# Kernel optimization log

Measured on AMD Instinct MI355X. Metric: run time of the kernel, lower is better.

Reference implementation:

```python
import jax, jax.numpy as jnp
import numpy as np

NUM_USERS = 1_000_000
NUM_AGES = 8
NUM_ATTR = 40
FACE_K = 64
VISUAL_DIM = 2048
HIDDEN = 512
BATCH = 16384
VOCAB = NUM_USERS + 24 + 2 + NUM_AGES + NUM_ATTR  # fm_linear input width


def setup_inputs() -> dict:
    key = jax.random.key(0)
    ks = jax.random.split(key, 24)
    s = 0.02
    inp = {
        "user_id": jax.random.randint(ks[0], (BATCH,), 0, NUM_USERS),
        "hour": jax.random.randint(ks[1], (BATCH,), 0, 24),
        "visual": jax.random.normal(ks[2], (BATCH, VISUAL_DIM), jnp.float32),
        "scale": jax.random.uniform(ks[3], (BATCH, 1), jnp.float32),
        "gender": jax.random.randint(ks[4], (BATCH,), 0, 2),
        "age": jax.random.randint(ks[5], (BATCH,), 0, NUM_AGES),
        "attribute": jax.random.randint(ks[6], (BATCH,), 0, NUM_ATTR),
        # embedding tables
        "user_emb": jax.random.normal(ks[7], (NUM_USERS, FACE_K), jnp.float32) * s,
        "hour_emb": jax.random.normal(ks[8], (24, FACE_K), jnp.float32) * s,
        "gender_emb": jax.random.normal(ks[9], (2, FACE_K), jnp.float32) * s,
        "age_emb": jax.random.normal(ks[10], (NUM_AGES, FACE_K), jnp.float32) * s,
        "attr_emb": jax.random.normal(ks[11], (NUM_ATTR, FACE_K), jnp.float32) * s,
        # visual linear
        "visu_w": jax.random.normal(ks[12], (FACE_K, VISUAL_DIM), jnp.float32) * s,
        "visu_b": jnp.zeros((FACE_K,), jnp.float32),
        # fm linear over concatenated one-hots (width VOCAB, out 2)
        "fm_w": jax.random.normal(ks[13], (2, VOCAB), jnp.float32) * s,
        "fm_b": jnp.zeros((2,), jnp.float32),
        # dnn
        "w1": jax.random.normal(ks[14], (HIDDEN, 6 * FACE_K), jnp.float32) * s,
        "b1": jnp.zeros((HIDDEN,), jnp.float32),
        "w2": jax.random.normal(ks[15], (HIDDEN, HIDDEN), jnp.float32) * s,
        "b2": jnp.zeros((HIDDEN,), jnp.float32),
        "w3": jax.random.normal(ks[16], (2, HIDDEN), jnp.float32) * s,
        "b3": jnp.zeros((2,), jnp.float32),
    }
    return inp


def reference(user_id, hour, visual, scale, gender, age, attribute,
              user_emb, hour_emb, gender_emb, age_emb, attr_emb,
              visu_w, visu_b, fm_w, fm_b, w1, b1, w2, b2, w3, b3):
    B = user_id.shape[0]
    # fm linear: one_hot @ W^T == gather-sum of W columns at the hot indices
    cols = jnp.stack([
        user_id,
        NUM_USERS + hour,
        NUM_USERS + 24 + gender,
        NUM_USERS + 24 + 2 + age,
        NUM_USERS + 24 + 2 + NUM_AGES + attribute,
    ], axis=1)  # [B, 5]
    linear_part = fm_w[:, cols].sum(axis=2).T + fm_b  # [B, 2]

    # embeddings
    user = user_emb[user_id]            # [B, K]
    hr = hour_emb[hour]                 # [B, K]
    face = jnp.stack([gender_emb[gender], attr_emb[attribute], age_emb[age]], axis=1)  # [B,3,K]
    face = scale[:, None, :] * jnp.tanh(face)  # scale [B,1] -> [B,1,1]
    embeddings = jnp.concatenate([user[:, None, :], hr[:, None, :], face], axis=1)  # [B,5,K]

    # FM second order
    so = jnp.square(embeddings.sum(axis=1)) - jnp.square(embeddings).sum(axis=1)  # [B,K]
    second_order = 0.5 * so.sum(axis=1)  # [B]
    fm = linear_part + second_order[:, None]  # [B,2]

    # DNN
    vis = visual @ visu_w.T + visu_b  # [B,K]
    x = jnp.concatenate([embeddings.reshape(B, 5 * FACE_K), vis], axis=1)  # [B,6K]
    x = jax.nn.relu(x @ w1.T + b1)
    x = jax.nn.relu(x @ w2.T + b2)
    x = x @ w3.T + b3
    return jax.nn.softmax(fm + x, axis=1)
```

## Files before the change

### kernel.cpp

```cpp
#include <hip/hip_runtime.h>
#include <hip/hip_bf16.h>
#include <stdint.h>

#define BATCH 16384
#define FACE_K 64
#define VISUAL_DIM 2048
#define HIDDEN 512
#define NUM_USERS 1000000
#define NUM_AGES 8
#define NUM_ATTR 40
#define VOCAB (NUM_USERS + 24 + 2 + NUM_AGES + NUM_ATTR)
#define XDIM 384

typedef __bf16 bf16x8 __attribute__((ext_vector_type(8)));
typedef float f32x4 __attribute__((ext_vector_type(4)));

__device__ __forceinline__ uint16_t f2bf(float f) {
    union { float f; uint32_t u; } v; v.f = f;
    uint32_t r = v.u + 0x7fffu + ((v.u >> 16) & 1u);
    return (uint16_t)(r >> 16);
}
__device__ __forceinline__ float bf2f(uint16_t h) {
    union { uint32_t u; float f; } v; v.u = ((uint32_t)h) << 16;
    return v.f;
}

__global__ void cvt_all(const float* __restrict__ visu_w, const float* __restrict__ w1,
                        const float* __restrict__ w2, uint16_t* __restrict__ vwb,
                        uint16_t* __restrict__ w1b, uint16_t* __restrict__ w2b) {
    int i = blockIdx.x * blockDim.x + threadIdx.x;
    const float4* src;
    ushort4* dst;
    if (i < 32768)       { src = (const float4*)visu_w + i;        dst = (ushort4*)vwb + i; }
    else if (i < 81920)  { src = (const float4*)w1 + (i - 32768);  dst = (ushort4*)w1b + (i - 32768); }
    else                 { src = (const float4*)w2 + (i - 81920);  dst = (ushort4*)w2b + (i - 81920); }
    float4 v = *src;
    ushort4 o;
    o.x = f2bf(v.x); o.y = f2bf(v.y); o.z = f2bf(v.z); o.w = f2bf(v.w);
    *dst = o;
}

#define VIS_BLOCKS 1024
__global__ __launch_bounds__(256) void front_kernel(
        const float* __restrict__ visual, const uint16_t* __restrict__ Wb,
        const float* __restrict__ bias,
        const int* __restrict__ uid, const int* __restrict__ hour,
        const float* __restrict__ scale, const int* __restrict__ gender,
        const int* __restrict__ age, const int* __restrict__ attr,
        const float* __restrict__ user_emb, const float* __restrict__ hour_emb,
        const float* __restrict__ gender_emb, const float* __restrict__ age_emb,
        const float* __restrict__ attr_emb,
        const float* __restrict__ fm_w, const float* __restrict__ fm_b,
        uint16_t* __restrict__ x, float* __restrict__ fm) {
    __shared__ float red[3 * 64 * 17];
    int t = threadIdx.x;
    int wv = t >> 6, lane = t & 63;

    if (blockIdx.x < VIS_BLOCKS) {
        int lc = lane & 15, quad = lane >> 4;
        int m0 = blockIdx.x * 16;
        const float*    ap = visual + (size_t)(m0 + lc) * VISUAL_DIM + wv * 512 + quad * 8;
        const uint16_t* wp = Wb + (size_t)lc * VISUAL_DIM + wv * 512 + quad * 8;

        f32x4 acc[4];
        #pragma unroll
        for (int j = 0; j < 4; ++j) acc[j] = (f32x4){0.f, 0.f, 0.f, 0.f};

        #pragma unroll 4
        for (int k = 0; k < 512; k += 32) {
            float4 a0 = *(const float4*)(ap + k);
            float4 a1 = *(const float4*)(ap + k + 4);
            bf16x8 af;
            af[0] = (__bf16)a0.x; af[1] = (__bf16)a0.y; af[2] = (__bf16)a0.z; af[3] = (__bf16)a0.w;
            af[4] = (__bf16)a1.x; af[5] = (__bf16)a1.y; af[6] = (__bf16)a1.z; af[7] = (__bf16)a1.w;
            #pragma unroll
            for (int j = 0; j < 4; ++j) {
                bf16x8 bf = *(const bf16x8*)(wp + (size_t)(j * 16) * VISUAL_DIM + k);
                acc[j] = __builtin_amdgcn_mfma_f32_16x16x32_bf16(af, bf, acc[j], 0, 0, 0);
            }
        }
        if (wv) {
            int base = (wv - 1) * 1088 + lane * 17;
            #pragma unroll
            for (int j = 0; j < 4; ++j)
                #pragma unroll
                for (int r = 0; r < 4; ++r)
                    red[base + j * 4 + r] = acc[j][r];
        }
        __syncthreads();
        if (wv == 0) {
            int base = lane * 17;
            #pragma unroll
            for (int j = 0; j < 4; ++j) {
                int col = j * 16 + lc;
                float b = bias[col];
                #pragma unroll
                for (int r = 0; r < 4; ++r) {
                    float sum = acc[j][r] + red[base + j * 4 + r]
                              + red[1088 + base + j * 4 + r] + red[2176 + base + j * 4 + r];
                    int row = m0 + quad * 4 + r;
                    x[(size_t)row * XDIM + 320 + col] = f2bf(sum + b);
                }
            }
        }
    } else {
        int row = (blockIdx.x - VIS_BLOCKS) * 4 + wv;
        int u = uid[row], h = hour[row], g = gender[row], a = age[row], at = attr[row];
        float sc = scale[row];
        float eu  = user_emb[(size_t)u * 64 + lane];
        float eh  = hour_emb[h * 64 + lane];
        float eg  = sc * tanhf(gender_emb[g * 64 + lane]);
        float eat = sc * tanhf(attr_emb[at * 64 + lane]);
        float eag = sc * tanhf(age_emb[a * 64 + lane]);
        float s  = eu + eh + eg + eat + eag;
        float sq = eu*eu + eh*eh + eg*eg + eat*eat + eag*eag;
        float so = s * s - sq;
        float l0 = 0.f, l1 = 0.f;
        if (lane < 5) {
            int col = (lane == 0) ? u
                    : (lane == 1) ? (NUM_USERS + h)
                    : (lane == 2) ? (NUM_USERS + 24 + g)
                    : (lane == 3) ? (NUM_USERS + 26 + a)
                    :               (NUM_USERS + 34 + at);
            l0 = fm_w[col];
            l1 = fm_w[VOCAB + col];
        }
        for (int m = 32; m; m >>= 1) {
            so += __shfl_xor(so, m);
            l0 += __shfl_xor(l0, m);
            l1 += __shfl_xor(l1, m);
        }
        if (lane == 0) {
            fm[row * 2 + 0] = l0 + fm_b[0] + 0.5f * so;
            fm[row * 2 + 1] = l1 + fm_b[1] + 0.5f * so;
        }
        size_t xb = (size_t)row * XDIM;
        x[xb +       lane] = f2bf(eu);
        x[xb +  64 + lane] = f2bf(eh);
        x[xb + 128 + lane] = f2bf(eg);
        x[xb + 192 + lane] = f2bf(eat);
        x[xb + 256 + lane] = f2bf(eag);
    }
}

template <int KTOT, bool RELU>
__global__ __launch_bounds__(256) void gemm32(const uint16_t* __restrict__ A,
                                              const uint16_t* __restrict__ W,
                                              const float* __restrict__ bias,
                                              uint16_t* __restrict__ C, int ldc) {
    int wv = threadIdx.x >> 6, lane = threadIdx.x & 63;
    int lc = lane & 15, quad = lane >> 4;
    int m0 = blockIdx.x * 128 + wv * 32;
    int n0 = blockIdx.y * 64;

    const uint16_t* ap0 = A + (size_t)(m0 + lc) * KTOT + quad * 8;
    const uint16_t* ap1 = ap0 + (size_t)16 * KTOT;
    const uint16_t* wp  = W + (size_t)(n0 + lc) * KTOT + quad * 8;

    f32x4 acc[2][4];
    #pragma unroll
    for (int i = 0; i < 2; ++i)
        #pragma unroll
        for (int j = 0; j < 4; ++j) acc[i][j] = (f32x4){0.f, 0.f, 0.f, 0.f};

    #pragma unroll 4
    for (int k = 0; k < KTOT; k += 32) {
        bf16x8 af0 = *(const bf16x8*)(ap0 + k);
        bf16x8 af1 = *(const bf16x8*)(ap1 + k);
        #pragma unroll
        for (int j = 0; j < 4; ++j) {
            bf16x8 bf = *(const bf16x8*)(wp + (size_t)(j * 16) * KTOT + k);
            acc[0][j] = __builtin_amdgcn_mfma_f32_16x16x32_bf16(af0, bf, acc[0][j], 0, 0, 0);
            acc[1][j] = __builtin_amdgcn_mfma_f32_16x16x32_bf16(af1, bf, acc[1][j], 0, 0, 0);
        }
    }
    #pragma unroll
    for (int j = 0; j < 4; ++j) {
        int col = n0 + j * 16 + lc;
        float b = bias[col];
        #pragma unroll
        for (int i = 0; i < 2; ++i) {
            #pragma unroll
            for (int r = 0; r < 4; ++r) {
                int row = m0 + i * 16 + quad * 4 + r;
                float v = acc[i][j][r] + b;
                if (RELU) v = fmaxf(v, 0.f);
                C[(size_t)row * ldc + col] = f2bf(v);
            }
        }
    }
}

__global__ void final_kernel(const uint16_t* __restrict__ h2, const float* __restrict__ w3,
                             const float* __restrict__ b3, const float* __restrict__ fm,
                             float* __restrict__ out) {
    int row = blockIdx.x * 4 + (threadIdx.x >> 6);
    int lane = threadIdx.x & 63;
    uint4 hv = *(const uint4*)(h2 + (size_t)row * HIDDEN + lane * 8);
    const uint16_t* hp = (const uint16_t*)&hv;
    float4 wa0 = *(const float4*)(w3 + lane * 8);
    float4 wb0 = *(const float4*)(w3 + lane * 8 + 4);
    float4 wa1 = *(const float4*)(w3 + HIDDEN + lane * 8);
    float4 wb1 = *(const float4*)(w3 + HIDDEN + lane * 8 + 4);
    float hf[8];
    #pragma unroll
    for (int j = 0; j < 8; ++j) hf[j] = bf2f(hp[j]);
    float d0 = hf[0]*wa0.x + hf[1]*wa0.y + hf[2]*wa0.z + hf[3]*wa0.w
             + hf[4]*wb0.x + hf[5]*wb0.y + hf[6]*wb0.z + hf[7]*wb0.w;
    float d1 = hf[0]*wa1.x + hf[1]*wa1.y + hf[2]*wa1.z + hf[3]*wa1.w
             + hf[4]*wb1.x + hf[5]*wb1.y + hf[6]*wb1.z + hf[7]*wb1.w;
    for (int m = 32; m; m >>= 1) {
        d0 += __shfl_xor(d0, m);
        d1 += __shfl_xor(d1, m);
    }
    if (lane == 0) {
        float l0 = fm[row * 2 + 0] + d0 + b3[0];
        float l1 = fm[row * 2 + 1] + d1 + b3[1];
        float mx = fmaxf(l0, l1);
        float e0 = __expf(l0 - mx), e1 = __expf(l1 - mx);
        float inv = 1.f / (e0 + e1);
        out[row * 2 + 0] = e0 * inv;
        out[row * 2 + 1] = e1 * inv;
    }
}

extern "C" void kernel_launch(void* const* d_in, const int* in_sizes, int n_in,
                              void* d_out, int out_size, void* d_ws, size_t ws_size,
                              hipStream_t stream) {
    const int*   user_id   = (const int*)d_in[0];
    const int*   hour      = (const int*)d_in[1];
    const float* visual    = (const float*)d_in[2];
    const float* scale     = (const float*)d_in[3];
    const int*   gender    = (const int*)d_in[4];
    const int*   age       = (const int*)d_in[5];
    const int*   attribute = (const int*)d_in[6];
    const float* user_emb  = (const float*)d_in[7];
    const float* hour_emb  = (const float*)d_in[8];
    const float* gender_emb= (const float*)d_in[9];
    const float* age_emb   = (const float*)d_in[10];
    const float* attr_emb  = (const float*)d_in[11];
    const float* visu_w    = (const float*)d_in[12];
    const float* visu_b    = (const float*)d_in[13];
    const float* fm_w      = (const float*)d_in[14];
    const float* fm_b      = (const float*)d_in[15];
    const float* w1        = (const float*)d_in[16];
    const float* b1        = (const float*)d_in[17];
    const float* w2        = (const float*)d_in[18];
    const float* b2        = (const float*)d_in[19];
    const float* w3        = (const float*)d_in[20];
    const float* b3        = (const float*)d_in[21];
    float* out = (float*)d_out;

    char* ws = (char*)d_ws;
    uint16_t* x   = (uint16_t*)ws;
    uint16_t* h1  = (uint16_t*)(ws + 12582912);
    uint16_t* h2  = (uint16_t*)(ws + 12582912 + 16777216);
    float*    fm  = (float*)   (ws + 12582912 + 2 * 16777216);
    uint16_t* vwb = (uint16_t*)(ws + 12582912 + 2 * 16777216 + 131072);
    uint16_t* w1b = vwb + 64 * 2048;
    uint16_t* w2b = w1b + 512 * 384;

    cvt_all<<<576, 256, 0, stream>>>(visu_w, w1, w2, vwb, w1b, w2b);
    front_kernel<<<VIS_BLOCKS + BATCH / 4, 256, 0, stream>>>(
        visual, vwb, visu_b,
        user_id, hour, scale, gender, age, attribute,
        user_emb, hour_emb, gender_emb, age_emb, attr_emb,
        fm_w, fm_b, x, fm);
    gemm32<XDIM, true><<<dim3(BATCH / 128, 8), 256, 0, stream>>>(x, w1b, b1, h1, HIDDEN);
    gemm32<HIDDEN, true><<<dim3(BATCH / 128, 8), 256, 0, stream>>>(h1, w2b, b2, h2, HIDDEN);
    final_kernel<<<BATCH / 4, 256, 0, stream>>>(h2, w3, b3, fm, out);
}
```

Baseline: 514.1 us.

## Fuse both DNN GEMMs and softmax head into one kernel via LDS

Replaces the two separate MFMA GEMM launches and the final softmax kernel with one kernel that computes 32 rows per block. The first-layer activations stay in LDS, and the second-layer output is reduced directly against w3. This removes the global round trips for the h1/h2 intermediates and two launches. In exchange, each block streams the full w1/w2 weights from cache for fewer rows, and occupancy drops because of high register and LDS use.

```diff
diff --git a/kernel.cpp b/kernel.cpp
--- a/kernel.cpp
+++ b/kernel.cpp
@@ -11,6 +11,7 @@
 #define NUM_ATTR 40
 #define VOCAB (NUM_USERS + 24 + 2 + NUM_AGES + NUM_ATTR)
 #define XDIM 384
+#define LDS_S 516
 
 typedef __bf16 bf16x8 __attribute__((ext_vector_type(8)));
 typedef float f32x4 __attribute__((ext_vector_type(4)));
@@ -143,84 +144,109 @@
     }
 }
 
-template <int KTOT, bool RELU>
-__global__ __launch_bounds__(256) void gemm32(const uint16_t* __restrict__ A,
-                                              const uint16_t* __restrict__ W,
-                                              const float* __restrict__ bias,
-                                              uint16_t* __restrict__ C, int ldc) {
-    int wv = threadIdx.x >> 6, lane = threadIdx.x & 63;
+__global__ __launch_bounds__(256) void fused_dnn(
+        const uint16_t* __restrict__ x, const uint16_t* __restrict__ w1b,
+        const float* __restrict__ b1, const uint16_t* __restrict__ w2b,
+        const float* __restrict__ b2, const float* __restrict__ w3,
+        const float* __restrict__ b3, const float* __restrict__ fm,
+        float* __restrict__ out) {
+    __shared__ uint16_t h1s[32 * LDS_S];
+    __shared__ float dred[2][16][2];
+    int t = threadIdx.x;
+    int wv = t >> 6, lane = t & 63;
+    int rg = wv >> 1, cs = wv & 1;
     int lc = lane & 15, quad = lane >> 4;
-    int m0 = blockIdx.x * 128 + wv * 32;
-    int n0 = blockIdx.y * 64;
-
-    const uint16_t* ap0 = A + (size_t)(m0 + lc) * KTOT + quad * 8;
-    const uint16_t* ap1 = ap0 + (size_t)16 * KTOT;
-    const uint16_t* wp  = W + (size_t)(n0 + lc) * KTOT + quad * 8;
-
-    f32x4 acc[2][4];
-    #pragma unroll
-    for (int i = 0; i < 2; ++i)
-        #pragma unroll
-        for (int j = 0; j < 4; ++j) acc[i][j] = (f32x4){0.f, 0.f, 0.f, 0.f};
-
-    #pragma unroll 4
-    for (int k = 0; k < KTOT; k += 32) {
-        bf16x8 af0 = *(const bf16x8*)(ap0 + k);
-        bf16x8 af1 = *(const bf16x8*)(ap1 + k);
-        #pragma unroll
-        for (int j = 0; j < 4; ++j) {
-            bf16x8 bf = *(const bf16x8*)(wp + (size_t)(j * 16) * KTOT + k);
-            acc[0][j] = __builtin_amdgcn_mfma_f32_16x16x32_bf16(af0, bf, acc[0][j], 0, 0, 0);
-            acc[1][j] = __builtin_amdgcn_mfma_f32_16x16x32_bf16(af1, bf, acc[1][j], 0, 0, 0);
-        }
-    }
-    #pragma unroll
-    for (int j = 0; j < 4; ++j) {
-        int col = n0 + j * 16 + lc;
-        float b = bias[col];
-        #pragma unroll
-        for (int i = 0; i < 2; ++i) {
-            #pragma unroll
-            for (int r = 0; r < 4; ++r) {
-                int row = m0 + i * 16 + quad * 4 + r;
-                float v = acc[i][j][r] + b;
-                if (RELU) v = fmaxf(v, 0.f);
-                C[(size_t)row * ldc + col] = f2bf(v);
-            }
-        }
-    }
-}
-
-__global__ void final_kernel(const uint16_t* __restrict__ h2, const float* __restrict__ w3,
-                             const float* __restrict__ b3, const float* __restrict__ fm,
-                             float* __restrict__ out) {
-    int row = blockIdx.x * 4 + (threadIdx.x >> 6);
-    int lane = threadIdx.x & 63;
-    uint4 hv = *(const uint4*)(h2 + (size_t)row * HIDDEN + lane * 8);
-    const uint16_t* hp = (const uint16_t*)&hv;
-    float4 wa0 = *(const float4*)(w3 + lane * 8);
-    float4 wb0 = *(const float4*)(w3 + lane * 8 + 4);
-    float4 wa1 = *(const float4*)(w3 + HIDDEN + lane * 8);
-    float4 wb1 = *(const float4*)(w3 + HIDDEN + lane * 8 + 4);
-    float hf[8];
-    #pragma unroll
-    for (int j = 0; j < 8; ++j) hf[j] = bf2f(hp[j]);
-    float d0 = hf[0]*wa0.x + hf[1]*wa0.y + hf[2]*wa0.z + hf[3]*wa0.w
-             + hf[4]*wb0.x + hf[5]*wb0.y + hf[6]*wb0.z + hf[7]*wb0.w;
-    float d1 = hf[0]*wa1.x + hf[1]*wa1.y + hf[2]*wa1.z + hf[3]*wa1.w
-             + hf[4]*wb1.x + hf[5]*wb1.y + hf[6]*wb1.z + hf[7]*wb1.w;
-    for (int m = 32; m; m >>= 1) {
-        d0 += __shfl_xor(d0, m);
-        d1 += __shfl_xor(d1, m);
-    }
-    if (lane == 0) {
-        float l0 = fm[row * 2 + 0] + d0 + b3[0];
-        float l1 = fm[row * 2 + 1] + d1 + b3[1];
-        float mx = fmaxf(l0, l1);
-        float e0 = __expf(l0 - mx), e1 = __expf(l1 - mx);
-        float inv = 1.f / (e0 + e1);
-        out[row * 2 + 0] = e0 * inv;
-        out[row * 2 + 1] = e1 * inv;
+    int m0 = blockIdx.x * 32 + rg * 16;
+
+    const uint16_t* ap  = x + (size_t)(m0 + lc) * XDIM + quad * 8;
+    const uint16_t* wp1 = w1b + (size_t)(cs * 256 + lc) * XDIM + quad * 8;
+
+    f32x4 acc[16];
+    #pragma unroll
+    for (int j = 0; j < 16; ++j) acc[j] = (f32x4){0.f, 0.f, 0.f, 0.f};
+
+    #pragma unroll 2
+    for (int ks = 0; ks < 12; ++ks) {
+        bf16x8 af = *(const bf16x8*)(ap + ks * 32);
+        #pragma unroll
+        for (int j = 0; j < 16; ++j) {
+            bf16x8 bf = *(const bf16x8*)(wp1 + (size_t)(j * 16) * XDIM + ks * 32);
+            acc[j] = __builtin_amdgcn_mfma_f32_16x16x32_bf16(af, bf, acc[j], 0, 0, 0);
+        }
+    }
+    #pragma unroll
+    for (int j = 0; j < 16; ++j) {
+        int col = cs * 256 + j * 16 + lc;
+        float bb = b1[col];
+        #pragma unroll
+        for (int r = 0; r < 4; ++r) {
+            float v = fmaxf(acc[j][r] + bb, 0.f);
+            h1s[(rg * 16 + quad * 4 + r) * LDS_S + col] = f2bf(v);
+        }
+    }
+    __syncthreads();
+
+    const uint16_t* lp  = h1s + (rg * 16 + lc) * LDS_S + quad * 8;
+    const uint16_t* wp2 = w2b + (size_t)(cs * 256 + lc) * HIDDEN + quad * 8;
+
+    f32x4 acc2[16];
+    #pragma unroll
+    for (int j = 0; j < 16; ++j) acc2[j] = (f32x4){0.f, 0.f, 0.f, 0.f};
+
+    #pragma unroll 2
+    for (int ks = 0; ks < 16; ++ks) {
+        union { bf16x8 v; ushort4 h[2]; } u;
+        u.h[0] = *(const ushort4*)(lp + ks * 32);
+        u.h[1] = *(const ushort4*)(lp + ks * 32 + 4);
+        bf16x8 af = u.v;
+        #pragma unroll
+        for (int j = 0; j < 16; ++j) {
+            bf16x8 bf = *(const bf16x8*)(wp2 + (size_t)(j * 16) * HIDDEN + ks * 32);
+            acc2[j] = __builtin_amdgcn_mfma_f32_16x16x32_bf16(af, bf, acc2[j], 0, 0, 0);
+        }
+    }
+
+    float d0[4] = {0.f, 0.f, 0.f, 0.f}, d1[4] = {0.f, 0.f, 0.f, 0.f};
+    #pragma unroll
+    for (int j = 0; j < 16; ++j) {
+        int col = cs * 256 + j * 16 + lc;
+        float bb = b2[col];
+        float wa = w3[col], wb2v = w3[HIDDEN + col];
+        #pragma unroll
+        for (int r = 0; r < 4; ++r) {
+            float v = fmaxf(acc2[j][r] + bb, 0.f);
+            d0[r] += v * wa;
+            d1[r] += v * wb2v;
+        }
+    }
+    #pragma unroll
+    for (int m = 1; m <= 8; m <<= 1) {
+        #pragma unroll
+        for (int r = 0; r < 4; ++r) {
+            d0[r] += __shfl_xor(d0[r], m);
+            d1[r] += __shfl_xor(d1[r], m);
+        }
+    }
+    if (cs == 1 && lc == 0) {
+        #pragma unroll
+        for (int r = 0; r < 4; ++r) {
+            dred[rg][quad * 4 + r][0] = d0[r];
+            dred[rg][quad * 4 + r][1] = d1[r];
+        }
+    }
+    __syncthreads();
+    if (cs == 0 && lc == 0) {
+        #pragma unroll
+        for (int r = 0; r < 4; ++r) {
+            int row = m0 + quad * 4 + r;
+            float l0 = fm[row * 2 + 0] + d0[r] + dred[rg][quad * 4 + r][0] + b3[0];
+            float l1 = fm[row * 2 + 1] + d1[r] + dred[rg][quad * 4 + r][1] + b3[1];
+            float mx = fmaxf(l0, l1);
+            float e0 = __expf(l0 - mx), e1 = __expf(l1 - mx);
+            float inv = 1.f / (e0 + e1);
+            out[row * 2 + 0] = e0 * inv;
+            out[row * 2 + 1] = e1 * inv;
+        }
     }
 }
 
@@ -253,10 +279,8 @@
 
     char* ws = (char*)d_ws;
     uint16_t* x   = (uint16_t*)ws;
-    uint16_t* h1  = (uint16_t*)(ws + 12582912);
-    uint16_t* h2  = (uint16_t*)(ws + 12582912 + 16777216);
-    float*    fm  = (float*)   (ws + 12582912 + 2 * 16777216);
-    uint16_t* vwb = (uint16_t*)(ws + 12582912 + 2 * 16777216 + 131072);
+    float*    fm  = (float*)   (ws + 12582912);
+    uint16_t* vwb = (uint16_t*)(ws + 12582912 + 131072);
     uint16_t* w1b = vwb + 64 * 2048;
     uint16_t* w2b = w1b + 512 * 384;
 
@@ -266,7 +290,5 @@
         user_id, hour, scale, gender, age, attribute,
         user_emb, hour_emb, gender_emb, age_emb, attr_emb,
         fm_w, fm_b, x, fm);
-    gemm32<XDIM, true><<<dim3(BATCH / 128, 8), 256, 0, stream>>>(x, w1b, b1, h1, HIDDEN);
-    gemm32<HIDDEN, true><<<dim3(BATCH / 128, 8), 256, 0, stream>>>(h1, w2b, b2, h2, HIDDEN);
-    final_kernel<<<BATCH / 4, 256, 0, stream>>>(h2, w3, b3, fm, out);
-}
+    fused_dnn<<<BATCH / 32, 256, 0, stream>>>(x, w1b, b1, w2b, b2, w3, b3, fm, out);
+}
```

Measured after the change: 534.1 us. 3.9% more time.
